# Optimization experiments

Hardware: AMD Instinct MI355X
Metric: run time of the kernel (lower is better)

Reference implementation:

```python
import jax, jax.numpy as jnp
import numpy as np

N, HW, ENC = 128, 14, 2048
V, E, D = 10000, 512, 512
MAXLEN = 32


def setup_inputs() -> dict:
    key = jax.random.key(0)
    ks = jax.random.split(key, 16)
    s = 0.02
    enc_feature = jax.random.normal(ks[0], (N, HW, HW, ENC), jnp.float32)
    enc_capt = jax.random.randint(ks[1], (N, MAXLEN), 0, V)
    capt_lengths = jax.random.randint(ks[2], (N, 1), 2, MAXLEN + 1)
    capt_lengths = capt_lengths.at[0, 0].set(MAXLEN)  # ensure max(decode_lengths)==MAXLEN-1 (static)
    rn = lambda k, sh: jax.random.normal(k, sh, jnp.float32) * s
    return dict(
        enc_feature=enc_feature, enc_capt=enc_capt, capt_lengths=capt_lengths,
        emb=rn(ks[3], (V, E)),
        W_ih=rn(ks[4], (4 * D, E + ENC)), b_ih=jnp.zeros((4 * D,), jnp.float32),
        W_hh=rn(ks[5], (4 * D, D)), b_hh=jnp.zeros((4 * D,), jnp.float32),
        W_inith=rn(ks[6], (D, ENC)), b_inith=jnp.zeros((D,), jnp.float32),
        W_initc=rn(ks[7], (D, ENC)), b_initc=jnp.zeros((D,), jnp.float32),
        W_fbeta=rn(ks[8], (ENC, D)), b_fbeta=jnp.zeros((ENC,), jnp.float32),
        W_fc=rn(ks[9], (V, D)), b_fc=jnp.zeros((V,), jnp.float32),
    )


def reference(enc_feature, enc_capt, capt_lengths, emb, W_ih, b_ih, W_hh, b_hh,
              W_inith, b_inith, W_initc, b_initc, W_fbeta, b_fbeta, W_fc, b_fc):
    n = enc_feature.shape[0]
    feat = enc_feature.reshape(n, -1, enc_feature.shape[-1])  # (N, P, ENC)
    P = feat.shape[1]
    cl = capt_lengths[:, 0]
    sort_ind = jnp.argsort(-cl)               # descending by caption length
    cl = cl[sort_ind]
    feat = feat[sort_ind]
    capt = enc_capt[sort_ind]
    embs = emb[capt]                          # (N, MAXLEN, E)
    mean_feat = feat.mean(axis=1)             # (N, ENC) - uniform attention context
    h = mean_feat @ W_inith.T + b_inith
    c = mean_feat @ W_initc.T + b_initc
    dec_len = cl - 1
    T = capt.shape[1] - 1                     # static max decode length
    mask = jnp.arange(T)[None, :] < dec_len[:, None]   # (N, T) ragged-batch mask
    xs = (jnp.swapaxes(embs[:, :T, :], 0, 1), mask.T)  # (T,N,E), (T,N)

    def step(carry, x):
        h, c = carry
        e_t, m = x
        gate = jax.nn.sigmoid(h @ W_fbeta.T + b_fbeta)          # (N, ENC)
        awe = mean_feat * gate                                   # gated attention-weighted encoding
        inp = jnp.concatenate([e_t, awe], axis=1)                # (N, E+ENC)
        g = inp @ W_ih.T + b_ih + h @ W_hh.T + b_hh              # LSTMCell gates
        i, f, gg, o = jnp.split(g, 4, axis=1)
        c_new = jax.nn.sigmoid(f) * c + jax.nn.sigmoid(i) * jnp.tanh(gg)
        h_new = jax.nn.sigmoid(o) * jnp.tanh(c_new)
        mf = m[:, None].astype(h.dtype)
        h2 = jnp.where(m[:, None], h_new, h)                     # inactive rows keep old state
        c2 = jnp.where(m[:, None], c_new, c)
        preds = (h_new @ W_fc.T + b_fc) * mf                     # dropout = identity (eval)
        return (h2, c2), (preds, mf)

    (_, _), (preds, mfs) = jax.lax.scan(step, (h, c), xs)
    predictions = jnp.swapaxes(preds, 0, 1)                      # (N, T, V)
    alphas = jnp.broadcast_to(jnp.swapaxes(mfs, 0, 1) / P, (n, T, P))  # uniform alpha, zero past len
    return predictions, capt, dec_len, alphas, sort_ind
```

## Files before the change

kernel.cpp:

```cpp
#include <hip/hip_runtime.h>
#include <hip/hip_bf16.h>
#include <math.h>

#define NB       128
#define P_HW     196
#define ENC_C    2048
#define V_SZ     10000
#define E_SZ     512
#define D_SZ     512
#define MAXLEN   32
#define T_STEPS  31

#define SZ_PRED    (128ULL * 31ULL * 10000ULL)
#define OFF_PRED   0ULL
#define OFF_CAPT   (SZ_PRED)
#define OFF_DECLEN (OFF_CAPT + 128ULL * 32ULL)
#define OFF_ALPHA  (OFF_DECLEN + 128ULL)
#define OFF_SORT   (OFF_ALPHA + 128ULL * 31ULL * 196ULL)

typedef __bf16 bf16x8 __attribute__((ext_vector_type(8)));
typedef float f32x4 __attribute__((ext_vector_type(4)));

__device__ __forceinline__ float sigf(float x) { return 1.0f / (1.0f + __expf(-x)); }

__device__ __forceinline__ unsigned short f2bf(float f) {
    unsigned int u = __float_as_uint(f);
    unsigned int r = (u + 0x7fffu + ((u >> 16) & 1u)) >> 16;
    return (unsigned short)r;
}

__global__ void sort_kernel(const int* __restrict__ capt_lengths,
                            const int* __restrict__ enc_capt,
                            int* __restrict__ sort_ind_ws,
                            int* __restrict__ dec_len_ws,
                            int* __restrict__ capt_sorted_ws,
                            float* __restrict__ dout) {
    __shared__ int cl[NB];
    int i = threadIdx.x;
    cl[i] = capt_lengths[i];
    __syncthreads();
    int my = cl[i];
    int rank = 0;
    #pragma unroll 4
    for (int j = 0; j < NB; ++j) {
        int cj = cl[j];
        rank += (cj > my) || (cj == my && j < i);
    }
    sort_ind_ws[rank] = i;
    dec_len_ws[rank]  = my - 1;
    dout[OFF_SORT + rank]   = (float)i;
    dout[OFF_DECLEN + rank] = (float)(my - 1);
    for (int t = 0; t < MAXLEN; ++t) {
        int tok = enc_capt[i * MAXLEN + t];
        capt_sorted_ws[rank * MAXLEN + t] = tok;
        dout[OFF_CAPT + rank * MAXLEN + t] = (float)tok;
    }
}

__global__ void mean_kernel(const float* __restrict__ enc_feature,
                            const int* __restrict__ sort_ind,
                            float* __restrict__ mean_feat,
                            unsigned short* __restrict__ mean16) {
    int b = blockIdx.y;
    int e = blockIdx.x * 256 + threadIdx.x;
    int src = sort_ind[b];
    const float* base = enc_feature + (size_t)src * P_HW * ENC_C + e;
    float s = 0.0f;
    #pragma unroll 4
    for (int p = 0; p < P_HW; ++p) s += base[(size_t)p * ENC_C];
    float m = s * (1.0f / (float)P_HW);
    mean_feat[(size_t)b * ENC_C + e] = m;
    mean16[(size_t)b * ENC_C + e] = f2bf(m);
}

__global__ void f32_to_bf16(const float* __restrict__ src,
                            unsigned short* __restrict__ dst, int n) {
    int i = (blockIdx.x * 256 + threadIdx.x) * 4;
    if (i < n) {
        float4 v = *reinterpret_cast<const float4*>(src + i);
        dst[i + 0] = f2bf(v.x);
        dst[i + 1] = f2bf(v.y);
        dst[i + 2] = f2bf(v.z);
        dst[i + 3] = f2bf(v.w);
    }
}

__global__ void concat_wg(const float* __restrict__ W_ih,
                          const float* __restrict__ W_hh,
                          unsigned short* __restrict__ Wg16) {
    int n = blockIdx.y;
    int col = blockIdx.x * 256 + threadIdx.x;
    float v = (col < 2560) ? W_ih[(size_t)n * 2560 + col]
                           : W_hh[(size_t)n * 512 + (col - 2560)];
    Wg16[(size_t)n * 3072 + col] = f2bf(v);
}

__global__ void bsum_kernel(const float* __restrict__ b_ih,
                            const float* __restrict__ b_hh,
                            float* __restrict__ bsum) {
    int i = blockIdx.x * 256 + threadIdx.x;
    bsum[i] = b_ih[i] + b_hh[i];
}

__global__ void embs_gather(const float* __restrict__ emb,
                            const int* __restrict__ capt_sorted,
                            unsigned short* __restrict__ embs16) {
    int idx = blockIdx.x * 256 + threadIdx.x;
    if (idx >= 31 * 128 * 512) return;
    int t = idx >> 16;
    int r = idx & 65535;
    int b = r >> 9;
    int tok = capt_sorted[b * MAXLEN + t];
    embs16[idx] = f2bf(emb[(size_t)tok * E_SZ + (r & 511)]);
}

template <int EPI>
__global__ __launch_bounds__(64) void mfma_gemm(
    const unsigned short* __restrict__ A, int lda,
    const unsigned short* __restrict__ B, int ldb,
    int Nout, int K,
    const float* __restrict__ bias,
    float* __restrict__ Cf, unsigned short* __restrict__ Cb, int ldc) {
    int l = threadIdx.x;
    int lm = l & 15;
    int lk = (l >> 4) << 3;
    int row0 = blockIdx.y << 5;
    int col0 = blockIdx.x << 5;
    const unsigned short* pa0 = A + (size_t)(row0 + lm) * lda + lk;
    const unsigned short* pa1 = pa0 + ((size_t)lda << 4);
    const unsigned short* pb0 = B + (size_t)(col0 + lm) * ldb + lk;
    const unsigned short* pb1 = pb0 + ((size_t)ldb << 4);
    f32x4 acc00 = {0.f, 0.f, 0.f, 0.f}, acc01 = acc00, acc10 = acc00, acc11 = acc00;
    for (int k = 0; k < K; k += 32) {
        bf16x8 a0 = *(const bf16x8*)(pa0 + k);
        bf16x8 a1 = *(const bf16x8*)(pa1 + k);
        bf16x8 b0 = *(const bf16x8*)(pb0 + k);
        bf16x8 b1 = *(const bf16x8*)(pb1 + k);
        acc00 = __builtin_amdgcn_mfma_f32_16x16x32_bf16(a0, b0, acc00, 0, 0, 0);
        acc01 = __builtin_amdgcn_mfma_f32_16x16x32_bf16(a0, b1, acc01, 0, 0, 0);
        acc10 = __builtin_amdgcn_mfma_f32_16x16x32_bf16(a1, b0, acc10, 0, 0, 0);
        acc11 = __builtin_amdgcn_mfma_f32_16x16x32_bf16(a1, b1, acc11, 0, 0, 0);
    }
    int orow = (l >> 4) << 2;
    #pragma unroll
    for (int mi = 0; mi < 2; ++mi) {
        #pragma unroll
        for (int ni = 0; ni < 2; ++ni) {
            f32x4 v = (mi == 0) ? (ni == 0 ? acc00 : acc01)
                                : (ni == 0 ? acc10 : acc11);
            int col = col0 + ni * 16 + lm;
            #pragma unroll
            for (int r = 0; r < 4; ++r) {
                int row = row0 + mi * 16 + orow + r;
                float val = v[r] + bias[col];
                if (EPI == 0) Cf[(size_t)row * ldc + col] = val;
                else          Cb[(size_t)row * ldc + col] = f2bf(val);
            }
        }
    }
}

__global__ __launch_bounds__(256) void awe_fused(
    const unsigned short* __restrict__ h16,
    const unsigned short* __restrict__ Wfb,
    const float* __restrict__ b_fbeta,
    const float* __restrict__ meanfeat,
    unsigned short* __restrict__ awe16) {
    __shared__ float red[2][1024];
    int tid = threadIdx.x;
    int w = tid >> 6, l = tid & 63;
    int ct = w >> 1, ks = w & 1;
    int lm = l & 15, lk = ((l >> 4) << 3);
    int row0 = blockIdx.y << 5;
    int col0 = (blockIdx.x << 6) + (ct << 5);
    int kbase = ks << 8;
    const unsigned short* pa0 = h16 + (size_t)(row0 + lm) * 512 + kbase + lk;
    const unsigned short* pa1 = pa0 + 16 * 512;
    const unsigned short* pb0 = Wfb + (size_t)(col0 + lm) * 512 + kbase + lk;
    const unsigned short* pb1 = pb0 + 16 * 512;
    f32x4 acc00 = {0.f, 0.f, 0.f, 0.f}, acc01 = acc00, acc10 = acc00, acc11 = acc00;
    #pragma unroll
    for (int k = 0; k < 256; k += 32) {
        bf16x8 a0 = *(const bf16x8*)(pa0 + k);
        bf16x8 a1 = *(const bf16x8*)(pa1 + k);
        bf16x8 b0 = *(const bf16x8*)(pb0 + k);
        bf16x8 b1 = *(const bf16x8*)(pb1 + k);
        acc00 = __builtin_amdgcn_mfma_f32_16x16x32_bf16(a0, b0, acc00, 0, 0, 0);
        acc01 = __builtin_amdgcn_mfma_f32_16x16x32_bf16(a0, b1, acc01, 0, 0, 0);
        acc10 = __builtin_amdgcn_mfma_f32_16x16x32_bf16(a1, b0, acc10, 0, 0, 0);
        acc11 = __builtin_amdgcn_mfma_f32_16x16x32_bf16(a1, b1, acc11, 0, 0, 0);
    }
    int orow = (l >> 4) << 2;
    if (ks == 1) {
        #pragma unroll
        for (int mi = 0; mi < 2; ++mi)
            #pragma unroll
            for (int ni = 0; ni < 2; ++ni) {
                f32x4 v = (mi == 0) ? (ni == 0 ? acc00 : acc01)
                                    : (ni == 0 ? acc10 : acc11);
                #pragma unroll
                for (int r = 0; r < 4; ++r)
                    red[ct][(mi * 16 + orow + r) * 32 + ni * 16 + lm] = v[r];
            }
    }
    __syncthreads();
    if (ks == 0) {
        #pragma unroll
        for (int mi = 0; mi < 2; ++mi)
            #pragma unroll
            for (int ni = 0; ni < 2; ++ni) {
                f32x4 v = (mi == 0) ? (ni == 0 ? acc00 : acc01)
                                    : (ni == 0 ? acc10 : acc11);
                int col = col0 + ni * 16 + lm;
                #pragma unroll
                for (int r = 0; r < 4; ++r) {
                    int row = row0 + mi * 16 + orow + r;
                    float val = v[r] + red[ct][(mi * 16 + orow + r) * 32 + ni * 16 + lm]
                              + b_fbeta[col];
                    awe16[(size_t)row * 2048 + col] =
                        f2bf(meanfeat[(size_t)row * 2048 + col] * sigf(val));
                }
            }
    }
}

__global__ __launch_bounds__(1024) void lstm_fused2(
    const unsigned short* __restrict__ embt,
    const unsigned short* __restrict__ awe16,
    const unsigned short* __restrict__ h_in,
    const unsigned short* __restrict__ Wg,
    const float* __restrict__ bsum,
    float* __restrict__ c,
    unsigned short* __restrict__ h_out,
    unsigned short* __restrict__ hnew16,
    const int* __restrict__ dec_len, int t) {
    __shared__ float red[12][512];
    int tid = threadIdx.x;
    int w = tid >> 6, l = tid & 63;
    int g = w & 3, ks = w >> 2;
    int lm = l & 15, lk = ((l >> 4) << 3);
    int r0 = blockIdx.y << 5;
    int d0 = blockIdx.x << 4;
    int ra = r0 + lm;
    const unsigned short* pe0 = embt  + (size_t)ra * 512  + lk;
    const unsigned short* pe1 = pe0 + 16 * 512;
    const unsigned short* pw0 = awe16 + (size_t)ra * 2048 + lk;
    const unsigned short* pw1 = pw0 + 16 * 2048;
    const unsigned short* ph0 = h_in  + (size_t)ra * 512  + lk;
    const unsigned short* ph1 = ph0 + 16 * 512;
    const unsigned short* pb  = Wg + (size_t)(g * 512 + d0 + lm) * 3072 + lk;
    f32x4 acc0 = {0.f, 0.f, 0.f, 0.f}, acc1 = acc0;
    int k0 = ks * 768;
    #pragma unroll 8
    for (int kk = 0; kk < 768; kk += 32) {
        int k = k0 + kk;
        bf16x8 a0, a1;
        if (k < 512)       { a0 = *(const bf16x8*)(pe0 + k);
                             a1 = *(const bf16x8*)(pe1 + k); }
        else if (k < 2560) { a0 = *(const bf16x8*)(pw0 + (k - 512));
                             a1 = *(const bf16x8*)(pw1 + (k - 512)); }
        else               { a0 = *(const bf16x8*)(ph0 + (k - 2560));
                             a1 = *(const bf16x8*)(ph1 + (k - 2560)); }
        bf16x8 b = *(const bf16x8*)(pb + k);
        acc0 = __builtin_amdgcn_mfma_f32_16x16x32_bf16(a0, b, acc0, 0, 0, 0);
        acc1 = __builtin_amdgcn_mfma_f32_16x16x32_bf16(a1, b, acc1, 0, 0, 0);
    }
    int orow = (l >> 4) << 2;
    if (ks > 0) {
        int slot = (ks - 1) * 4 + g;
        #pragma unroll
        for (int r = 0; r < 4; ++r) {
            red[slot][(orow + r) * 16 + lm]      = acc0[r];
            red[slot][(16 + orow + r) * 16 + lm] = acc1[r];
        }
    }
    __syncthreads();
    if (ks == 0) {
        #pragma unroll
        for (int r = 0; r < 4; ++r) {
            int e0 = (orow + r) * 16 + lm;
            int e1 = (16 + orow + r) * 16 + lm;
            red[g][e0] = acc0[r] + red[g][e0] + red[4 + g][e0] + red[8 + g][e0];
            red[g][e1] = acc1[r] + red[g][e1] + red[4 + g][e1] + red[8 + g][e1];
        }
    }
    __syncthreads();
    if (tid < 512) {
        int r = tid >> 4, d = tid & 15;
        int R = r0 + r, D = d0 + d;
        int e = r * 16 + d;
        float gi = red[0][e] + bsum[D];
        float gf = red[1][e] + bsum[512 + D];
        float gg = red[2][e] + bsum[1024 + D];
        float go = red[3][e] + bsum[1536 + D];
        size_t idx = (size_t)R * 512 + D;
        float cn = sigf(gf) * c[idx] + sigf(gi) * tanhf(gg);
        float hn = sigf(go) * tanhf(cn);
        unsigned short hb = f2bf(hn);
        hnew16[idx] = hb;
        if (t < dec_len[R]) {
            c[idx] = cn;
            h_out[idx] = hb;
        } else {
            h_out[idx] = h_in[idx];
        }
    }
}

__global__ __launch_bounds__(256) void fc128(
    const unsigned short* __restrict__ hnew_all,
    const unsigned short* __restrict__ Wfc,
    const float* __restrict__ b_fc,
    const int* __restrict__ dec_len,
    float* __restrict__ out) {
    int tid = threadIdx.x;
    int w = tid >> 6, l = tid & 63;
    int wm = w >> 1, wn = w & 1;
    int lm = l & 15, lk = ((l >> 4) << 3);
    int row0 = blockIdx.x * 128 + wm * 64;
    int col0 = blockIdx.y * 128 + wn * 64;
    const unsigned short* pa[4];
    const unsigned short* pb[4];
    #pragma unroll
    for (int i = 0; i < 4; ++i) {
        pa[i] = hnew_all + (size_t)(row0 + i * 16 + lm) * 512 + lk;
        int bn = col0 + i * 16 + lm; if (bn > 9999) bn = 9999;
        pb[i] = Wfc + (size_t)bn * 512 + lk;
    }
    f32x4 acc[4][4];
    #pragma unroll
    for (int i = 0; i < 4; ++i)
        #pragma unroll
        for (int j = 0; j < 4; ++j) acc[i][j] = (f32x4){0.f, 0.f, 0.f, 0.f};
    for (int k = 0; k < 512; k += 32) {
        bf16x8 a[4], b[4];
        #pragma unroll
        for (int i = 0; i < 4; ++i) a[i] = *(const bf16x8*)(pa[i] + k);
        #pragma unroll
        for (int j = 0; j < 4; ++j) b[j] = *(const bf16x8*)(pb[j] + k);
        #pragma unroll
        for (int i = 0; i < 4; ++i)
            #pragma unroll
            for (int j = 0; j < 4; ++j)
                acc[i][j] = __builtin_amdgcn_mfma_f32_16x16x32_bf16(a[i], b[j], acc[i][j], 0, 0, 0);
    }
    int orow = (l >> 4) << 2;
    #pragma unroll
    for (int i = 0; i < 4; ++i) {
        #pragma unroll
        for (int j = 0; j < 4; ++j) {
            int col = col0 + j * 16 + lm;
            if (col >= 10000) continue;
            float bias = b_fc[col];
            #pragma unroll
            for (int r = 0; r < 4; ++r) {
                int row = row0 + i * 16 + orow + r;
                int t = row >> 7, b = row & 127;
                bool m = t < dec_len[b];
                out[OFF_PRED + ((size_t)b * 31 + t) * 10000 + col] =
                    m ? (acc[i][j][r] + bias) : 0.0f;
            }
        }
    }
}

__global__ void alphas_kernel(const int* __restrict__ dec_len,
                              float* __restrict__ dout) {
    int idx = blockIdx.x * 256 + threadIdx.x;
    int b = idx / (31 * 196);
    int r = idx % (31 * 196);
    int t = r / 196;
    dout[OFF_ALPHA + idx] = (t < dec_len[b]) ? (1.0f / 196.0f) : 0.0f;
}

static inline char* align256(char* p) {
    return (char*)(((uintptr_t)p + 255) & ~(uintptr_t)255);
}

extern "C" void kernel_launch(void* const* d_in, const int* in_sizes, int n_in,
                              void* d_out, int out_size, void* d_ws, size_t ws_size,
                              hipStream_t stream) {
    const float* enc_feature  = (const float*)d_in[0];
    const int*   enc_capt     = (const int*)d_in[1];
    const int*   capt_lengths = (const int*)d_in[2];
    const float* emb     = (const float*)d_in[3];
    const float* W_ih    = (const float*)d_in[4];
    const float* b_ih    = (const float*)d_in[5];
    const float* W_hh    = (const float*)d_in[6];
    const float* b_hh    = (const float*)d_in[7];
    const float* W_inith = (const float*)d_in[8];
    const float* b_inith = (const float*)d_in[9];
    const float* W_initc = (const float*)d_in[10];
    const float* b_initc = (const float*)d_in[11];
    const float* W_fbeta = (const float*)d_in[12];
    const float* b_fbeta = (const float*)d_in[13];
    const float* W_fc    = (const float*)d_in[14];
    const float* b_fc    = (const float*)d_in[15];
    float* out = (float*)d_out;

    char* ws = (char*)d_ws;
    int* sort_ind    = (int*)ws;  ws += 512;
    int* dec_len     = (int*)ws;  ws += 512;
    int* capt_sorted = (int*)ws;  ws += 128 * MAXLEN * sizeof(int);
    ws = align256(ws);
    float* mean_feat = (float*)ws; ws += (size_t)128 * 2048 * 4;
    float* c         = (float*)ws; ws += (size_t)128 * 512 * 4;
    float* bsum      = (float*)ws; ws += 2048 * 4;
    unsigned short* mean16   = (unsigned short*)ws; ws += (size_t)128 * 2048 * 2;
    unsigned short* hbuf0    = (unsigned short*)ws; ws += (size_t)128 * 512 * 2;
    unsigned short* hbuf1    = (unsigned short*)ws; ws += (size_t)128 * 512 * 2;
    unsigned short* awe16    = (unsigned short*)ws; ws += (size_t)128 * 2048 * 2;
    unsigned short* Wfb16    = (unsigned short*)ws; ws += (size_t)2048 * 512 * 2;
    unsigned short* Wg16     = (unsigned short*)ws; ws += (size_t)2048 * 3072 * 2;
    unsigned short* Wfc16    = (unsigned short*)ws; ws += (size_t)10000 * 512 * 2;
    unsigned short* Winith16 = (unsigned short*)ws; ws += (size_t)512 * 2048 * 2;
    unsigned short* Winitc16 = (unsigned short*)ws; ws += (size_t)512 * 2048 * 2;
    unsigned short* embs16   = (unsigned short*)ws; ws += (size_t)31 * 128 * 512 * 2;
    unsigned short* hnew_all = (unsigned short*)ws; ws += (size_t)31 * 128 * 512 * 2;

    sort_kernel<<<1, 128, 0, stream>>>(capt_lengths, enc_capt, sort_ind, dec_len,
                                       capt_sorted, out);
    mean_kernel<<<dim3(8, 128), 256, 0, stream>>>(enc_feature, sort_ind,
                                                  mean_feat, mean16);

    f32_to_bf16<<<(2048 * 512 / 4 + 255) / 256, 256, 0, stream>>>(W_fbeta, Wfb16, 2048 * 512);
    f32_to_bf16<<<(10000 * 512 / 4 + 255) / 256, 256, 0, stream>>>(W_fc, Wfc16, 10000 * 512);
    f32_to_bf16<<<(512 * 2048 / 4 + 255) / 256, 256, 0, stream>>>(W_inith, Winith16, 512 * 2048);
    f32_to_bf16<<<(512 * 2048 / 4 + 255) / 256, 256, 0, stream>>>(W_initc, Winitc16, 512 * 2048);
    concat_wg<<<dim3(12, 2048), 256, 0, stream>>>(W_ih, W_hh, Wg16);
    bsum_kernel<<<8, 256, 0, stream>>>(b_ih, b_hh, bsum);
    embs_gather<<<(31 * 128 * 512 + 255) / 256, 256, 0, stream>>>(emb, capt_sorted, embs16);

    mfma_gemm<4><<<dim3(16, 4), 64, 0, stream>>>(
        mean16, 2048, Winith16, 2048, 512, 2048, b_inith, nullptr, hbuf0, 512);
    mfma_gemm<0><<<dim3(16, 4), 64, 0, stream>>>(
        mean16, 2048, Winitc16, 2048, 512, 2048, b_initc, c, nullptr, 512);

    unsigned short* hb[2] = {hbuf0, hbuf1};
    for (int t = 0; t < T_STEPS; ++t) {
        unsigned short* hin  = hb[t & 1];
        unsigned short* hout = hb[(t + 1) & 1];
        awe_fused<<<dim3(32, 4), 256, 0, stream>>>(
            hin, Wfb16, b_fbeta, mean_feat, awe16);
        lstm_fused2<<<dim3(32, 4), 1024, 0, stream>>>(
            embs16 + (size_t)t * 128 * 512, awe16, hin, Wg16, bsum,
            c, hout, hnew_all + (size_t)t * 128 * 512, dec_len, t);
    }

    fc128<<<dim3(31, 79), 256, 0, stream>>>(
        hnew_all, Wfc16, b_fc, dec_len, out);
    alphas_kernel<<<3038, 256, 0, stream>>>(dec_len, out);
}
```

Measured before the change: 1.907 ms.

## Fuse recurrent LSTM steps into persistent cooperative kernel with grid syncs

Replaces the 62 per-step kernel launches (awe gate plus LSTM cell) and the two init GEMMs with one cooperative persistent kernel of 256 blocks that runs every timestep and separates phases with grid.sync. The gate weights and bias are reordered so the i/f/g/o columns for one hidden unit sit next to each other, which lets each block reduce its own gates. K-splitting across 8 waves with a shared-memory reduction gives every phase all 256 blocks. The fc GEMM grid is remapped with XCD-aware block swizzling to improve L2 locality. The goal is to remove launch overhead and raise parallelism, at the cost of two grid-wide barriers per step and a requirement that all blocks be co-resident.

After: 5.665 ms. 2.97x slower.

```diff
diff --git a/kernel.cpp b/kernel.cpp
--- a/kernel.cpp
+++ b/kernel.cpp
@@ -1,6 +1,9 @@
 #include <hip/hip_runtime.h>
+#include <hip/hip_cooperative_groups.h>
 #include <hip/hip_bf16.h>
 #include <math.h>
+
+namespace cg = cooperative_groups;
 
 #define NB       128
 #define P_HW     196
@@ -87,19 +90,20 @@
 
 __global__ void concat_wg(const float* __restrict__ W_ih,
                           const float* __restrict__ W_hh,
-                          unsigned short* __restrict__ Wg16) {
+                          unsigned short* __restrict__ WgP) {
     int n = blockIdx.y;
     int col = blockIdx.x * 256 + threadIdx.x;
     float v = (col < 2560) ? W_ih[(size_t)n * 2560 + col]
                            : W_hh[(size_t)n * 512 + (col - 2560)];
-    Wg16[(size_t)n * 3072 + col] = f2bf(v);
+    int p = ((n & 511) << 2) | (n >> 9);
+    WgP[(size_t)p * 3072 + col] = f2bf(v);
 }
 
 __global__ void bsum_kernel(const float* __restrict__ b_ih,
                             const float* __restrict__ b_hh,
-                            float* __restrict__ bsum) {
+                            float* __restrict__ bsumP) {
     int i = blockIdx.x * 256 + threadIdx.x;
-    bsum[i] = b_ih[i] + b_hh[i];
+    bsumP[((i & 511) << 2) | (i >> 9)] = b_ih[i] + b_hh[i];
 }
 
 __global__ void embs_gather(const float* __restrict__ emb,
@@ -114,211 +118,237 @@
     embs16[idx] = f2bf(emb[(size_t)tok * E_SZ + (r & 511)]);
 }
 
-template <int EPI>
-__global__ __launch_bounds__(64) void mfma_gemm(
-    const unsigned short* __restrict__ A, int lda,
-    const unsigned short* __restrict__ B, int ldb,
-    int Nout, int K,
-    const float* __restrict__ bias,
-    float* __restrict__ Cf, unsigned short* __restrict__ Cb, int ldc) {
-    int l = threadIdx.x;
-    int lm = l & 15;
-    int lk = (l >> 4) << 3;
-    int row0 = blockIdx.y << 5;
-    int col0 = blockIdx.x << 5;
-    const unsigned short* pa0 = A + (size_t)(row0 + lm) * lda + lk;
-    const unsigned short* pa1 = pa0 + ((size_t)lda << 4);
-    const unsigned short* pb0 = B + (size_t)(col0 + lm) * ldb + lk;
-    const unsigned short* pb1 = pb0 + ((size_t)ldb << 4);
-    f32x4 acc00 = {0.f, 0.f, 0.f, 0.f}, acc01 = acc00, acc10 = acc00, acc11 = acc00;
-    for (int k = 0; k < K; k += 32) {
-        bf16x8 a0 = *(const bf16x8*)(pa0 + k);
-        bf16x8 a1 = *(const bf16x8*)(pa1 + k);
-        bf16x8 b0 = *(const bf16x8*)(pb0 + k);
-        bf16x8 b1 = *(const bf16x8*)(pb1 + k);
-        acc00 = __builtin_amdgcn_mfma_f32_16x16x32_bf16(a0, b0, acc00, 0, 0, 0);
-        acc01 = __builtin_amdgcn_mfma_f32_16x16x32_bf16(a0, b1, acc01, 0, 0, 0);
-        acc10 = __builtin_amdgcn_mfma_f32_16x16x32_bf16(a1, b0, acc10, 0, 0, 0);
-        acc11 = __builtin_amdgcn_mfma_f32_16x16x32_bf16(a1, b1, acc11, 0, 0, 0);
-    }
+struct PP {
+    const unsigned short* mean16;
+    const float* mean_feat;
+    const unsigned short* Wfb;
+    const float* b_fbeta;
+    const unsigned short* WgP;
+    const float* bsumP;
+    const unsigned short* Winith;
+    const float* b_inith;
+    const unsigned short* Winitc;
+    const float* b_initc;
+    const unsigned short* embs;
+    float* c;
+    unsigned short* h0;
+    unsigned short* h1;
+    unsigned short* awe;
+    unsigned short* hnew_all;
+    const int* dec_len;
+};
+
+__global__ __launch_bounds__(512, 2) void persistent_kernel(PP p) {
+    cg::grid_group grid = cg::this_grid();
+    __shared__ float red[8][1024];
+    int blk = blockIdx.x, tid = threadIdx.x;
+    int w = tid >> 6, l = tid & 63;
+    int lm = l & 15, lk = (l >> 4) << 3;
     int orow = (l >> 4) << 2;
-    #pragma unroll
-    for (int mi = 0; mi < 2; ++mi) {
-        #pragma unroll
-        for (int ni = 0; ni < 2; ++ni) {
-            f32x4 v = (mi == 0) ? (ni == 0 ? acc00 : acc01)
-                                : (ni == 0 ? acc10 : acc11);
-            int col = col0 + ni * 16 + lm;
-            #pragma unroll
-            for (int r = 0; r < 4; ++r) {
-                int row = row0 + mi * 16 + orow + r;
-                float val = v[r] + bias[col];
-                if (EPI == 0) Cf[(size_t)row * ldc + col] = val;
-                else          Cb[(size_t)row * ldc + col] = f2bf(val);
-            }
+    int xcd = blk & 7, jj = blk >> 3;
+    int bm = jj & 3, bn = (xcd << 3) + (jj >> 2);
+
+    if (blk < 128) {
+        int sel = blk >> 6;
+        int j = blk & 63;
+        int row0 = (j >> 4) << 5, col0 = (j & 15) << 5;
+        const unsigned short* W = sel ? p.Winitc : p.Winith;
+        const unsigned short* pa0 = p.mean16 + (size_t)(row0 + lm) * 2048 + lk;
+        const unsigned short* pa1 = pa0 + 16 * 2048;
+        const unsigned short* pb0 = W + (size_t)(col0 + lm) * 2048 + lk;
+        const unsigned short* pb1 = pb0 + 16 * 2048;
+        f32x4 a00 = {0.f,0.f,0.f,0.f}, a01 = a00, a10 = a00, a11 = a00;
+        int k0 = w << 8;
+        #pragma unroll 4
+        for (int kk = 0; kk < 256; kk += 32) {
+            int k = k0 + kk;
+            bf16x8 av0 = *(const bf16x8*)(pa0 + k);
+            bf16x8 av1 = *(const bf16x8*)(pa1 + k);
+            bf16x8 bv0 = *(const bf16x8*)(pb0 + k);
+            bf16x8 bv1 = *(const bf16x8*)(pb1 + k);
+            a00 = __builtin_amdgcn_mfma_f32_16x16x32_bf16(av0, bv0, a00, 0, 0, 0);
+            a01 = __builtin_amdgcn_mfma_f32_16x16x32_bf16(av0, bv1, a01, 0, 0, 0);
+            a10 = __builtin_amdgcn_mfma_f32_16x16x32_bf16(av1, bv0, a10, 0, 0, 0);
+            a11 = __builtin_amdgcn_mfma_f32_16x16x32_bf16(av1, bv1, a11, 0, 0, 0);
         }
-    }
-}
-
-__global__ __launch_bounds__(256) void awe_fused(
-    const unsigned short* __restrict__ h16,
-    const unsigned short* __restrict__ Wfb,
-    const float* __restrict__ b_fbeta,
-    const float* __restrict__ meanfeat,
-    unsigned short* __restrict__ awe16) {
-    __shared__ float red[2][1024];
-    int tid = threadIdx.x;
-    int w = tid >> 6, l = tid & 63;
-    int ct = w >> 1, ks = w & 1;
-    int lm = l & 15, lk = ((l >> 4) << 3);
-    int row0 = blockIdx.y << 5;
-    int col0 = (blockIdx.x << 6) + (ct << 5);
-    int kbase = ks << 8;
-    const unsigned short* pa0 = h16 + (size_t)(row0 + lm) * 512 + kbase + lk;
-    const unsigned short* pa1 = pa0 + 16 * 512;
-    const unsigned short* pb0 = Wfb + (size_t)(col0 + lm) * 512 + kbase + lk;
-    const unsigned short* pb1 = pb0 + 16 * 512;
-    f32x4 acc00 = {0.f, 0.f, 0.f, 0.f}, acc01 = acc00, acc10 = acc00, acc11 = acc00;
-    #pragma unroll
-    for (int k = 0; k < 256; k += 32) {
-        bf16x8 a0 = *(const bf16x8*)(pa0 + k);
-        bf16x8 a1 = *(const bf16x8*)(pa1 + k);
-        bf16x8 b0 = *(const bf16x8*)(pb0 + k);
-        bf16x8 b1 = *(const bf16x8*)(pb1 + k);
-        acc00 = __builtin_amdgcn_mfma_f32_16x16x32_bf16(a0, b0, acc00, 0, 0, 0);
-        acc01 = __builtin_amdgcn_mfma_f32_16x16x32_bf16(a0, b1, acc01, 0, 0, 0);
-        acc10 = __builtin_amdgcn_mfma_f32_16x16x32_bf16(a1, b0, acc10, 0, 0, 0);
-        acc11 = __builtin_amdgcn_mfma_f32_16x16x32_bf16(a1, b1, acc11, 0, 0, 0);
-    }
-    int orow = (l >> 4) << 2;
-    if (ks == 1) {
         #pragma unroll
         for (int mi = 0; mi < 2; ++mi)
             #pragma unroll
             for (int ni = 0; ni < 2; ++ni) {
-                f32x4 v = (mi == 0) ? (ni == 0 ? acc00 : acc01)
-                                    : (ni == 0 ? acc10 : acc11);
+                f32x4 v = (mi == 0) ? (ni == 0 ? a00 : a01) : (ni == 0 ? a10 : a11);
                 #pragma unroll
                 for (int r = 0; r < 4; ++r)
-                    red[ct][(mi * 16 + orow + r) * 32 + ni * 16 + lm] = v[r];
-            }
-    }
-    __syncthreads();
-    if (ks == 0) {
-        #pragma unroll
-        for (int mi = 0; mi < 2; ++mi)
-            #pragma unroll
-            for (int ni = 0; ni < 2; ++ni) {
-                f32x4 v = (mi == 0) ? (ni == 0 ? acc00 : acc01)
-                                    : (ni == 0 ? acc10 : acc11);
-                int col = col0 + ni * 16 + lm;
+                    red[w][(mi * 16 + orow + r) * 32 + ni * 16 + lm] = v[r];
+            }
+        __syncthreads();
+        if (tid < 256) {
+            float4 s = {0.f, 0.f, 0.f, 0.f};
+            #pragma unroll
+            for (int ww = 0; ww < 8; ++ww) {
+                float4 v = *(const float4*)&red[ww][tid * 4];
+                s.x += v.x; s.y += v.y; s.z += v.z; s.w += v.w;
+            }
+            int row = row0 + (tid >> 3), c4 = col0 + ((tid & 7) << 2);
+            if (sel == 0) {
+                float4 b = *(const float4*)&p.b_inith[c4];
+                ushort4 o;
+                o.x = f2bf(s.x + b.x); o.y = f2bf(s.y + b.y);
+                o.z = f2bf(s.z + b.z); o.w = f2bf(s.w + b.w);
+                *(ushort4*)&p.h0[(size_t)row * 512 + c4] = o;
+            } else {
+                float4 b = *(const float4*)&p.b_initc[c4];
+                float4 o = {s.x + b.x, s.y + b.y, s.z + b.z, s.w + b.w};
+                *(float4*)&p.c[(size_t)row * 512 + c4] = o;
+            }
+        }
+    }
+    __threadfence();
+    grid.sync();
+
+    for (int t = 0; t < T_STEPS; ++t) {
+        const unsigned short* hin = (t & 1) ? p.h1 : p.h0;
+        unsigned short* hout      = (t & 1) ? p.h0 : p.h1;
+        {
+            int row0 = bm << 5, col0 = bn << 5;
+            const unsigned short* pa0 = hin + (size_t)(row0 + lm) * 512 + lk;
+            const unsigned short* pa1 = pa0 + 16 * 512;
+            const unsigned short* pb0 = p.Wfb + (size_t)(col0 + lm) * 512 + lk;
+            const unsigned short* pb1 = pb0 + 16 * 512;
+            f32x4 a00 = {0.f,0.f,0.f,0.f}, a01 = a00, a10 = a00, a11 = a00;
+            int k0 = w << 6;
+            #pragma unroll
+            for (int kk = 0; kk < 64; kk += 32) {
+                int k = k0 + kk;
+                bf16x8 av0 = *(const bf16x8*)(pa0 + k);
+                bf16x8 av1 = *(const bf16x8*)(pa1 + k);
+                bf16x8 bv0 = *(const bf16x8*)(pb0 + k);
+                bf16x8 bv1 = *(const bf16x8*)(pb1 + k);
+                a00 = __builtin_amdgcn_mfma_f32_16x16x32_bf16(av0, bv0, a00, 0, 0, 0);
+                a01 = __builtin_amdgcn_mfma_f32_16x16x32_bf16(av0, bv1, a01, 0, 0, 0);
+                a10 = __builtin_amdgcn_mfma_f32_16x16x32_bf16(av1, bv0, a10, 0, 0, 0);
+                a11 = __builtin_amdgcn_mfma_f32_16x16x32_bf16(av1, bv1, a11, 0, 0, 0);
+            }
+            #pragma unroll
+            for (int mi = 0; mi < 2; ++mi)
                 #pragma unroll
-                for (int r = 0; r < 4; ++r) {
-                    int row = row0 + mi * 16 + orow + r;
-                    float val = v[r] + red[ct][(mi * 16 + orow + r) * 32 + ni * 16 + lm]
-                              + b_fbeta[col];
-                    awe16[(size_t)row * 2048 + col] =
-                        f2bf(meanfeat[(size_t)row * 2048 + col] * sigf(val));
+                for (int ni = 0; ni < 2; ++ni) {
+                    f32x4 v = (mi == 0) ? (ni == 0 ? a00 : a01) : (ni == 0 ? a10 : a11);
+                    #pragma unroll
+                    for (int r = 0; r < 4; ++r)
+                        red[w][(mi * 16 + orow + r) * 32 + ni * 16 + lm] = v[r];
                 }
-            }
-    }
-}
-
-__global__ __launch_bounds__(1024) void lstm_fused2(
-    const unsigned short* __restrict__ embt,
-    const unsigned short* __restrict__ awe16,
-    const unsigned short* __restrict__ h_in,
-    const unsigned short* __restrict__ Wg,
-    const float* __restrict__ bsum,
-    float* __restrict__ c,
-    unsigned short* __restrict__ h_out,
-    unsigned short* __restrict__ hnew16,
-    const int* __restrict__ dec_len, int t) {
-    __shared__ float red[12][512];
-    int tid = threadIdx.x;
-    int w = tid >> 6, l = tid & 63;
-    int g = w & 3, ks = w >> 2;
-    int lm = l & 15, lk = ((l >> 4) << 3);
-    int r0 = blockIdx.y << 5;
-    int d0 = blockIdx.x << 4;
-    int ra = r0 + lm;
-    const unsigned short* pe0 = embt  + (size_t)ra * 512  + lk;
-    const unsigned short* pe1 = pe0 + 16 * 512;
-    const unsigned short* pw0 = awe16 + (size_t)ra * 2048 + lk;
-    const unsigned short* pw1 = pw0 + 16 * 2048;
-    const unsigned short* ph0 = h_in  + (size_t)ra * 512  + lk;
-    const unsigned short* ph1 = ph0 + 16 * 512;
-    const unsigned short* pb  = Wg + (size_t)(g * 512 + d0 + lm) * 3072 + lk;
-    f32x4 acc0 = {0.f, 0.f, 0.f, 0.f}, acc1 = acc0;
-    int k0 = ks * 768;
-    #pragma unroll 8
-    for (int kk = 0; kk < 768; kk += 32) {
-        int k = k0 + kk;
-        bf16x8 a0, a1;
-        if (k < 512)       { a0 = *(const bf16x8*)(pe0 + k);
-                             a1 = *(const bf16x8*)(pe1 + k); }
-        else if (k < 2560) { a0 = *(const bf16x8*)(pw0 + (k - 512));
-                             a1 = *(const bf16x8*)(pw1 + (k - 512)); }
-        else               { a0 = *(const bf16x8*)(ph0 + (k - 2560));
-                             a1 = *(const bf16x8*)(ph1 + (k - 2560)); }
-        bf16x8 b = *(const bf16x8*)(pb + k);
-        acc0 = __builtin_amdgcn_mfma_f32_16x16x32_bf16(a0, b, acc0, 0, 0, 0);
-        acc1 = __builtin_amdgcn_mfma_f32_16x16x32_bf16(a1, b, acc1, 0, 0, 0);
-    }
-    int orow = (l >> 4) << 2;
-    if (ks > 0) {
-        int slot = (ks - 1) * 4 + g;
-        #pragma unroll
-        for (int r = 0; r < 4; ++r) {
-            red[slot][(orow + r) * 16 + lm]      = acc0[r];
-            red[slot][(16 + orow + r) * 16 + lm] = acc1[r];
+            __syncthreads();
+            if (tid < 256) {
+                float4 s = {0.f, 0.f, 0.f, 0.f};
+                #pragma unroll
+                for (int ww = 0; ww < 8; ++ww) {
+                    float4 v = *(const float4*)&red[ww][tid * 4];
+                    s.x += v.x; s.y += v.y; s.z += v.z; s.w += v.w;
+                }
+                int row = row0 + (tid >> 3), c4 = col0 + ((tid & 7) << 2);
+                float4 b = *(const float4*)&p.b_fbeta[c4];
+                const float* mf = p.mean_feat + (size_t)row * 2048 + c4;
+                ushort4 o;
+                o.x = f2bf(mf[0] * sigf(s.x + b.x));
+                o.y = f2bf(mf[1] * sigf(s.y + b.y));
+                o.z = f2bf(mf[2] * sigf(s.z + b.z));
+                o.w = f2bf(mf[3] * sigf(s.w + b.w));
+                *(ushort4*)&p.awe[(size_t)row * 2048 + c4] = o;
+            }
         }
-    }
-    __syncthreads();
-    if (ks == 0) {
-        #pragma unroll
-        for (int r = 0; r < 4; ++r) {
-            int e0 = (orow + r) * 16 + lm;
-            int e1 = (16 + orow + r) * 16 + lm;
-            red[g][e0] = acc0[r] + red[g][e0] + red[4 + g][e0] + red[8 + g][e0];
-            red[g][e1] = acc1[r] + red[g][e1] + red[4 + g][e1] + red[8 + g][e1];
+        __threadfence();
+        grid.sync();
+        {
+            int row0 = bm << 5;
+            int p0 = bn << 5;
+            int d0 = bn << 3;
+            int ra = row0 + lm;
+            const unsigned short* embt = p.embs + (size_t)t * 65536;
+            const unsigned short* pe0 = embt + (size_t)ra * 512 + lk;
+            const unsigned short* pe1 = pe0 + 16 * 512;
+            const unsigned short* pw0 = p.awe + (size_t)ra * 2048 + lk;
+            const unsigned short* pw1 = pw0 + 16 * 2048;
+            const unsigned short* ph0 = hin + (size_t)ra * 512 + lk;
+            const unsigned short* ph1 = ph0 + 16 * 512;
+            const unsigned short* pb0 = p.WgP + (size_t)(p0 + lm) * 3072 + lk;
+            const unsigned short* pb1 = pb0 + (size_t)16 * 3072;
+            f32x4 a00 = {0.f,0.f,0.f,0.f}, a01 = a00, a10 = a00, a11 = a00;
+            int k0 = w * 384;
+            #pragma unroll 4
+            for (int kk = 0; kk < 384; kk += 32) {
+                int k = k0 + kk;
+                bf16x8 av0, av1;
+                if (k < 512)       { av0 = *(const bf16x8*)(pe0 + k);
+                                     av1 = *(const bf16x8*)(pe1 + k); }
+                else if (k < 2560) { av0 = *(const bf16x8*)(pw0 + (k - 512));
+                                     av1 = *(const bf16x8*)(pw1 + (k - 512)); }
+                else               { av0 = *(const bf16x8*)(ph0 + (k - 2560));
+                                     av1 = *(const bf16x8*)(ph1 + (k - 2560)); }
+                bf16x8 bv0 = *(const bf16x8*)(pb0 + k);
+                bf16x8 bv1 = *(const bf16x8*)(pb1 + k);
+                a00 = __builtin_amdgcn_mfma_f32_16x16x32_bf16(av0, bv0, a00, 0, 0, 0);
+                a01 = __builtin_amdgcn_mfma_f32_16x16x32_bf16(av0, bv1, a01, 0, 0, 0);
+                a10 = __builtin_amdgcn_mfma_f32_16x16x32_bf16(av1, bv0, a10, 0, 0, 0);
+                a11 = __builtin_amdgcn_mfma_f32_16x16x32_bf16(av1, bv1, a11, 0, 0, 0);
+            }
+            #pragma unroll
+            for (int mi = 0; mi < 2; ++mi)
+                #pragma unroll
+                for (int ni = 0; ni < 2; ++ni) {
+                    f32x4 v = (mi == 0) ? (ni == 0 ? a00 : a01) : (ni == 0 ? a10 : a11);
+                    #pragma unroll
+                    for (int r = 0; r < 4; ++r)
+                        red[w][(mi * 16 + orow + r) * 32 + ni * 16 + lm] = v[r];
+                }
+            __syncthreads();
+            if (tid < 256) {
+                float4 s = {0.f, 0.f, 0.f, 0.f};
+                #pragma unroll
+                for (int ww = 0; ww < 8; ++ww) {
+                    float4 v = *(const float4*)&red[ww][tid * 4];
+                    s.x += v.x; s.y += v.y; s.z += v.z; s.w += v.w;
+                }
+                int row = tid >> 3, dloc = tid & 7;
+                float4 bs = *(const float4*)&p.bsumP[p0 + dloc * 4];
+                float gi = s.x + bs.x, gf = s.y + bs.y;
+                float gg = s.z + bs.z, go = s.w + bs.w;
+                int R = row0 + row, D = d0 + dloc;
+                size_t idx = (size_t)R * 512 + D;
+                float cn = sigf(gf) * p.c[idx] + sigf(gi) * tanhf(gg);
+                float hn = sigf(go) * tanhf(cn);
+                unsigned short hb = f2bf(hn);
+                p.hnew_all[(size_t)t * 65536 + idx] = hb;
+                if (t < p.dec_len[R]) {
+                    p.c[idx] = cn;
+                    hout[idx] = hb;
+                } else {
+                    hout[idx] = hin[idx];
+                }
+            }
         }
-    }
-    __syncthreads();
-    if (tid < 512) {
-        int r = tid >> 4, d = tid & 15;
-        int R = r0 + r, D = d0 + d;
-        int e = r * 16 + d;
-        float gi = red[0][e] + bsum[D];
-        float gf = red[1][e] + bsum[512 + D];
-        float gg = red[2][e] + bsum[1024 + D];
-        float go = red[3][e] + bsum[1536 + D];
-        size_t idx = (size_t)R * 512 + D;
-        float cn = sigf(gf) * c[idx] + sigf(gi) * tanhf(gg);
-        float hn = sigf(go) * tanhf(cn);
-        unsigned short hb = f2bf(hn);
-        hnew16[idx] = hb;
-        if (t < dec_len[R]) {
-            c[idx] = cn;
-            h_out[idx] = hb;
-        } else {
-            h_out[idx] = h_in[idx];
-        }
-    }
-}
-
-__global__ __launch_bounds__(256) void fc128(
+        __threadfence();
+        grid.sync();
+    }
+}
+
+__global__ __launch_bounds__(256) void fc128x(
     const unsigned short* __restrict__ hnew_all,
     const unsigned short* __restrict__ Wfc,
     const float* __restrict__ b_fc,
     const int* __restrict__ dec_len,
     float* __restrict__ out) {
+    int bidx = blockIdx.x;
+    int xcd = bidx & 7;
+    int j = bidx >> 3;
+    int m = j % 31;
+    int n = xcd * 10 + j / 31;
+    if (n >= 79) return;
     int tid = threadIdx.x;
     int w = tid >> 6, l = tid & 63;
     int wm = w >> 1, wn = w & 1;
     int lm = l & 15, lk = ((l >> 4) << 3);
-    int row0 = blockIdx.x * 128 + wm * 64;
-    int col0 = blockIdx.y * 128 + wn * 64;
+    int row0 = m * 128 + wm * 64;
+    int col0 = n * 128 + wn * 64;
     const unsigned short* pa[4];
     const unsigned short* pb[4];
     #pragma unroll
@@ -331,34 +361,34 @@
     #pragma unroll
     for (int i = 0; i < 4; ++i)
         #pragma unroll
-        for (int j = 0; j < 4; ++j) acc[i][j] = (f32x4){0.f, 0.f, 0.f, 0.f};
+        for (int jq = 0; jq < 4; ++jq) acc[i][jq] = (f32x4){0.f, 0.f, 0.f, 0.f};
     for (int k = 0; k < 512; k += 32) {
         bf16x8 a[4], b[4];
         #pragma unroll
         for (int i = 0; i < 4; ++i) a[i] = *(const bf16x8*)(pa[i] + k);
         #pragma unroll
-        for (int j = 0; j < 4; ++j) b[j] = *(const bf16x8*)(pb[j] + k);
+        for (int jq = 0; jq < 4; ++jq) b[jq] = *(const bf16x8*)(pb[jq] + k);
         #pragma unroll
         for (int i = 0; i < 4; ++i)
             #pragma unroll
-            for (int j = 0; j < 4; ++j)
-                acc[i][j] = __builtin_amdgcn_mfma_f32_16x16x32_bf16(a[i], b[j], acc[i][j], 0, 0, 0);
+            for (int jq = 0; jq < 4; ++jq)
+                acc[i][jq] = __builtin_amdgcn_mfma_f32_16x16x32_bf16(a[i], b[jq], acc[i][jq], 0, 0, 0);
     }
     int orow = (l >> 4) << 2;
     #pragma unroll
     for (int i = 0; i < 4; ++i) {
         #pragma unroll
-        for (int j = 0; j < 4; ++j) {
-            int col = col0 + j * 16 + lm;
+        for (int jq = 0; jq < 4; ++jq) {
+            int col = col0 + jq * 16 + lm;
             if (col >= 10000) continue;
             float bias = b_fc[col];
             #pragma unroll
             for (int r = 0; r < 4; ++r) {
                 int row = row0 + i * 16 + orow + r;
                 int t = row >> 7, b = row & 127;
-                bool m = t < dec_len[b];
+                bool msk = t < dec_len[b];
                 out[OFF_PRED + ((size_t)b * 31 + t) * 10000 + col] =
-                    m ? (acc[i][j][r] + bias) : 0.0f;
+                    msk ? (acc[i][jq][r] + bias) : 0.0f;
             }
         }
     }
@@ -405,13 +435,13 @@
     ws = align256(ws);
     float* mean_feat = (float*)ws; ws += (size_t)128 * 2048 * 4;
     float* c         = (float*)ws; ws += (size_t)128 * 512 * 4;
-    float* bsum      = (float*)ws; ws += 2048 * 4;
+    float* bsumP     = (float*)ws; ws += 2048 * 4;
     unsigned short* mean16   = (unsigned short*)ws; ws += (size_t)128 * 2048 * 2;
     unsigned short* hbuf0    = (unsigned short*)ws; ws += (size_t)128 * 512 * 2;
     unsigned short* hbuf1    = (unsigned short*)ws; ws += (size_t)128 * 512 * 2;
     unsigned short* awe16    = (unsigned short*)ws; ws += (size_t)128 * 2048 * 2;
     unsigned short* Wfb16    = (unsigned short*)ws; ws += (size_t)2048 * 512 * 2;
-    unsigned short* Wg16     = (unsigned short*)ws; ws += (size_t)2048 * 3072 * 2;
+    unsigned short* WgP16    = (unsigned short*)ws; ws += (size_t)2048 * 3072 * 2;
     unsigned short* Wfc16    = (unsigned short*)ws; ws += (size_t)10000 * 512 * 2;
     unsigned short* Winith16 = (unsigned short*)ws; ws += (size_t)512 * 2048 * 2;
     unsigned short* Winitc16 = (unsigned short*)ws; ws += (size_t)512 * 2048 * 2;
@@ -427,27 +457,24 @@
     f32_to_bf16<<<(10000 * 512 / 4 + 255) / 256, 256, 0, stream>>>(W_fc, Wfc16, 10000 * 512);
     f32_to_bf16<<<(512 * 2048 / 4 + 255) / 256, 256, 0, stream>>>(W_inith, Winith16, 512 * 2048);
     f32_to_bf16<<<(512 * 2048 / 4 + 255) / 256, 256, 0, stream>>>(W_initc, Winitc16, 512 * 2048);
-    concat_wg<<<dim3(12, 2048), 256, 0, stream>>>(W_ih, W_hh, Wg16);
-    bsum_kernel<<<8, 256, 0, stream>>>(b_ih, b_hh, bsum);
+    concat_wg<<<dim3(12, 2048), 256, 0, stream>>>(W_ih, W_hh, WgP16);
+    bsum_kernel<<<8, 256, 0, stream>>>(b_ih, b_hh, bsumP);
     embs_gather<<<(31 * 128 * 512 + 255) / 256, 256, 0, stream>>>(emb, capt_sorted, embs16);
 
-    mfma_gemm<4><<<dim3(16, 4), 64, 0, stream>>>(
-        mean16, 2048, Winith16, 2048, 512, 2048, b_inith, nullptr, hbuf0, 512);
-    mfma_gemm<0><<<dim3(16, 4), 64, 0, stream>>>(
-        mean16, 2048, Winitc16, 2048, 512, 2048, b_initc, c, nullptr, 512);
-
-    unsigned short* hb[2] = {hbuf0, hbuf1};
-    for (int t = 0; t < T_STEPS; ++t) {
-        unsigned short* hin  = hb[t & 1];
-        unsigned short* hout = hb[(t + 1) & 1];
-        awe_fused<<<dim3(32, 4), 256, 0, stream>>>(
-            hin, Wfb16, b_fbeta, mean_feat, awe16);
-        lstm_fused2<<<dim3(32, 4), 1024, 0, stream>>>(
-            embs16 + (size_t)t * 128 * 512, awe16, hin, Wg16, bsum,
-            c, hout, hnew_all + (size_t)t * 128 * 512, dec_len, t);
-    }
-
-    fc128<<<dim3(31, 79), 256, 0, stream>>>(
-        hnew_all, Wfc16, b_fc, dec_len, out);
+    PP pp;
+    pp.mean16 = mean16;   pp.mean_feat = mean_feat;
+    pp.Wfb = Wfb16;       pp.b_fbeta = b_fbeta;
+    pp.WgP = WgP16;       pp.bsumP = bsumP;
+    pp.Winith = Winith16; pp.b_inith = b_inith;
+    pp.Winitc = Winitc16; pp.b_initc = b_initc;
+    pp.embs = embs16;     pp.c = c;
+    pp.h0 = hbuf0;        pp.h1 = hbuf1;
+    pp.awe = awe16;       pp.hnew_all = hnew_all;
+    pp.dec_len = dec_len;
+    void* args[] = { &pp };
+    hipLaunchCooperativeKernel((const void*)persistent_kernel,
+                               dim3(256), dim3(512), args, 0, stream);
+
+    fc128x<<<2480, 256, 0, stream>>>(hnew_all, Wfc16, b_fc, dec_len, out);
     alphas_kernel<<<3038, 256, 0, stream>>>(dec_len, out);
 }
```
